# Kernel tuning notes

Hardware: AMD Instinct MI355X
Metric: run time of the kernel (lower is better)

The kernel has to match this reference:

```python
import jax, jax.numpy as jnp
import numpy as np

# SSMBlock constants (from init_kwargs and standard mamba_ssm defaults)
W = 8            # pooled spatial edge; d_model = W^3
K = 16           # AvgPool3d kernel & stride
D_MODEL = W ** 3            # 512
D_STATE = 16
EXPAND = 2
D_INNER = EXPAND * D_MODEL  # 1024
DT_RANK = D_MODEL // 16     # 32 (ceil(512/16))
D_CONV = 4


def setup_inputs() -> dict:
    key = jax.random.key(0)
    ks = jax.random.split(key, 8)
    s = 0.02
    x = jax.random.normal(ks[0], (1, 64, 128, 128, 128), dtype=jnp.float32)
    in_proj_w = jax.random.normal(ks[1], (2 * D_INNER, D_MODEL), jnp.float32) * s
    conv_w = jax.random.normal(ks[2], (D_INNER, D_CONV), jnp.float32) * s
    conv_b = jnp.zeros((D_INNER,), jnp.float32)
    x_proj_w = jax.random.normal(ks[3], (DT_RANK + 2 * D_STATE, D_INNER), jnp.float32) * s
    dt_proj_w = jax.random.normal(ks[4], (D_INNER, DT_RANK), jnp.float32) * s
    dt_proj_b = jax.random.uniform(ks[5], (D_INNER,), jnp.float32, minval=-4.0, maxval=-2.0)
    A_log = jnp.log(jnp.broadcast_to(jnp.arange(1, D_STATE + 1, dtype=jnp.float32), (D_INNER, D_STATE)))
    D = jnp.ones((D_INNER,), jnp.float32)
    out_proj_w = jax.random.normal(ks[6], (D_MODEL, D_INNER), jnp.float32) * s
    return dict(x=x, in_proj_w=in_proj_w, conv_w=conv_w, conv_b=conv_b,
                x_proj_w=x_proj_w, dt_proj_w=dt_proj_w, dt_proj_b=dt_proj_b,
                A_log=A_log, D=D, out_proj_w=out_proj_w)


def _forward(x, in_proj_w, conv_w, conv_b, x_proj_w, dt_proj_w, dt_proj_b, A_log, D, out_proj_w):
    B, C = x.shape[0], x.shape[1]
    # AvgPool3d(K, stride=K): non-overlapping -> reshape + mean
    xp = x.reshape(B, C, W, K, W, K, W, K).mean(axis=(3, 5, 7))  # (B,C,W,W,W)
    seq = xp.reshape(B, C, D_MODEL)  # Mamba input: L = C, d_model = W^3

    # in_proj -> (x, z)
    xz = jnp.einsum('bld,ed->ble', seq, in_proj_w)  # (B,L,2*D_INNER)
    xs, z = jnp.split(xz, 2, axis=-1)

    # causal depthwise conv1d along L + SiLU
    xt = jnp.pad(xs, ((0, 0), (D_CONV - 1, 0), (0, 0))).transpose(0, 2, 1)  # (B,E,L+pad)
    conv = jax.lax.conv_general_dilated(
        xt, conv_w[:, None, :], window_strides=(1,), padding='VALID',
        dimension_numbers=('NCH', 'OIH', 'NCH'), feature_group_count=D_INNER)
    xs = jax.nn.silu(conv.transpose(0, 2, 1) + conv_b)  # (B,L,E)

    # input-dependent dt, B, C
    x_dbl = jnp.einsum('ble,fe->blf', xs, x_proj_w)
    dt, Bs, Cs = jnp.split(x_dbl, [DT_RANK, DT_RANK + D_STATE], axis=-1)
    dt = jax.nn.softplus(jnp.einsum('blr,er->ble', dt, dt_proj_w) + dt_proj_b)  # (B,L,E)

    # selective scan: h_t = exp(dt*A) h_{t-1} + (dt*x) B_t ; y_t = <h_t, C_t> + D*x_t
    A = -jnp.exp(A_log)                                  # (E,S)
    dA = jnp.exp(dt[..., None] * A)                      # (B,L,E,S)
    dBx = (dt * xs)[..., None] * Bs[:, :, None, :]       # (B,L,E,S)

    def step(h, inp):
        da, dbx, c = inp
        h = da * h + dbx                                 # (B,E,S)
        y = jnp.einsum('bes,bs->be', h, c)
        return h, y

    h0 = jnp.zeros((B, D_INNER, D_STATE), xs.dtype)
    _, ys = jax.lax.scan(step, h0, (dA.transpose(1, 0, 2, 3), dBx.transpose(1, 0, 2, 3), Cs.transpose(1, 0, 2)))
    y = ys.transpose(1, 0, 2) + xs * D                   # (B,L,E)

    y = y * jax.nn.silu(z)
    out = jnp.einsum('ble,de->bld', y, out_proj_w)       # (B,L,d_model)
    return out.reshape(B, C, W, W, W)


def reference(x, in_proj_w, conv_w, conv_b, x_proj_w, dt_proj_w, dt_proj_b, A_log, D, out_proj_w):
    return _forward(x, in_proj_w, conv_w, conv_b, x_proj_w, dt_proj_w, dt_proj_b, A_log, D, out_proj_w)
```

## Files before the change

kernel.cpp:

```cpp
#include <hip/hip_runtime.h>
#include <math.h>

typedef float f32x4 __attribute__((ext_vector_type(4)));

__device__ __forceinline__ float dot4v(f32x4 a, f32x4 b){
    return a.x*b.x + a.y*b.y + a.z*b.z + a.w*b.w;
}
__device__ __forceinline__ float dot4(float4 a, float4 b){
    return a.x*b.x + a.y*b.y + a.z*b.z + a.w*b.w;
}

__device__ __forceinline__ float reduce4(float a0, float a1, float a2, float a3, int lane){
    int b0 = lane & 1, b1 = lane & 2;
    float r  = b0 ? a1 : a0;
    float rt = b0 ? a0 : a1;
    r += __shfl_xor(rt, 1);
    float s  = b0 ? a3 : a2;
    float st = b0 ? a2 : a3;
    s += __shfl_xor(st, 1);
    float u  = b1 ? s : r;
    float ut = b1 ? r : s;
    u += __shfl_xor(ut, 2);
    u += __shfl_xor(u, 4);
    u += __shfl_xor(u, 8);
    u += __shfl_xor(u, 16);
    u += __shfl_xor(u, 32);
    return u;
}

__global__ __launch_bounds__(256) void pool_k(const float* __restrict__ x,
                                              float* __restrict__ seq){
    __shared__ float red[4][8];
    int tid  = threadIdx.x;
    int lane = tid & 63;
    int part = tid >> 6;
    int cdh  = blockIdx.x;
    int c  = cdh >> 6;
    int od = (cdh >> 3) & 7;
    int oh = cdh & 7;
    int half = lane >> 5;
    int f    = lane & 31;

    const f32x4* px = (const f32x4*)x;
    size_t base = ((size_t)(c * 128 + od * 16) * 128 + (size_t)(oh * 16 + half)) * 32 + f
                + (size_t)part * 4 * 4096;

    float acc = 0.f;
    #pragma unroll
    for (int ii = 0; ii < 4; ii++){
        size_t o = base + (size_t)ii * 4096;
        #pragma unroll
        for (int jj = 0; jj < 8; jj++){
            f32x4 v = __builtin_nontemporal_load(&px[o + (size_t)jj * 64]);
            acc += (v.x + v.y) + (v.z + v.w);
        }
    }
    acc += __shfl_xor(acc, 1);
    acc += __shfl_xor(acc, 2);
    acc += __shfl_xor(acc, 32);
    if (lane < 32 && (lane & 3) == 0) red[part][lane >> 2] = acc;
    __syncthreads();
    if (tid < 8){
        float v = red[0][tid] + red[1][tid] + red[2][tid] + red[3][tid];
        seq[c * 512 + od * 64 + oh * 8 + tid] = v * (1.0f / 4096.0f);
    }
}

__global__ __launch_bounds__(256) void inproj_k(const float* __restrict__ seq,
                                                const float* __restrict__ Win,
                                                float* __restrict__ xz){
    int lane = threadIdx.x & 63;
    int wid  = blockIdx.x * 4 + (threadIdx.x >> 6);
    int l0 = (wid >> 8) << 4;
    int e0 = (wid & 255) << 3;
    const f32x4* S = (const f32x4*)seq;
    f32x4 sa[16], sb[16];
    #pragma unroll
    for (int r = 0; r < 16; r++){
        sa[r] = S[(size_t)(l0 + r) * 128 + lane];
        sb[r] = S[(size_t)(l0 + r) * 128 + lane + 64];
    }
    #pragma unroll 2
    for (int j = 0; j < 8; j++){
        int e = e0 + j;
        const f32x4* W = (const f32x4*)Win + (size_t)e * 128;
        f32x4 w0 = W[lane], w1 = W[lane + 64];
        float a[16];
        #pragma unroll
        for (int r = 0; r < 16; r++) a[r] = dot4v(w0, sa[r]) + dot4v(w1, sb[r]);
        float u0 = reduce4(a[0],  a[1],  a[2],  a[3],  lane);
        float u1 = reduce4(a[4],  a[5],  a[6],  a[7],  lane);
        float u2 = reduce4(a[8],  a[9],  a[10], a[11], lane);
        float u3 = reduce4(a[12], a[13], a[14], a[15], lane);
        if (lane < 4){
            xz[(size_t)(l0 + lane) * 2048 + e]      = u0;
            xz[(size_t)(l0 + 4  + lane) * 2048 + e] = u1;
            xz[(size_t)(l0 + 8  + lane) * 2048 + e] = u2;
            xz[(size_t)(l0 + 12 + lane) * 2048 + e] = u3;
        }
    }
}

__global__ __launch_bounds__(256) void xpc_k(const float* __restrict__ xz,
                                             const float* __restrict__ cw,
                                             const float* __restrict__ cb,
                                             const float* __restrict__ Wx,
                                             float* __restrict__ xsT,
                                             float* __restrict__ zsT,
                                             float* __restrict__ bcT,
                                             float* __restrict__ xdT){
    __shared__ float xs_row[1024];
    int bid = blockIdx.x;
    int l  = bid >> 2;
    int fg = bid & 3;
    int t  = threadIdx.x;

    #pragma unroll
    for (int j = 0; j < 4; j++){
        int e = t + j * 256;
        float v = cb[e];
        #pragma unroll
        for (int tt = 0; tt < 4; tt++){
            int ll = l - 3 + tt;
            if (ll >= 0) v += cw[e * 4 + tt] * xz[(size_t)ll * 2048 + e];
        }
        v = v / (1.f + expf(-v));
        xs_row[e] = v;
        if (fg == 0){
            xsT[(size_t)e * 64 + l] = v;
            float zv = xz[(size_t)l * 2048 + 1024 + e];
            zsT[(size_t)e * 64 + l] = zv / (1.f + expf(-zv));
        }
    }
    __syncthreads();

    int f = fg * 16 + (t >> 4);
    int q = t & 15;
    const float4* X  = (const float4*)xs_row;
    const float4* W4 = (const float4*)(Wx + (size_t)f * 1024);
    float acc = 0.f;
    #pragma unroll
    for (int k4 = 0; k4 < 16; k4++){
        int idx = q * 16 + k4;
        acc += dot4(X[idx], W4[idx]);
    }
    acc += __shfl_xor(acc, 1);
    acc += __shfl_xor(acc, 2);
    acc += __shfl_xor(acc, 4);
    acc += __shfl_xor(acc, 8);
    if (q == 0){
        if (f < 32) xdT[(size_t)f * 64 + l] = acc;
        else        bcT[(size_t)(f - 32) * 64 + l] = acc;
    }
}

__global__ __launch_bounds__(256) void scan_k(const float* __restrict__ xdT,
                                              const float* __restrict__ bcT,
                                              const float* __restrict__ xsT,
                                              const float* __restrict__ zsT,
                                              const float* __restrict__ Wdt,
                                              const float* __restrict__ bdt,
                                              const float* __restrict__ A_log,
                                              const float* __restrict__ Dv,
                                              float* __restrict__ y){
    __shared__ float red[4][64];
    int e    = blockIdx.x;
    int lane = threadIdx.x & 63;
    int w    = threadIdx.x >> 6;

    float acc = bdt[e];
    #pragma unroll 8
    for (int k = 0; k < 32; k++) acc += xdT[k * 64 + lane] * Wdt[e * 32 + k];
    float dtv = (acc > 20.f) ? acc : log1pf(expf(acc));
    float xv  = xsT[(size_t)e * 64 + lane];

    float py = 0.f;
    #pragma unroll
    for (int i = 0; i < 4; i++){
        int s = w * 4 + i;
        float A = -expf(A_log[e * 16 + s]);
        float a = expf(dtv * A);
        float b = (dtv * xv) * bcT[s * 64 + lane];
        #pragma unroll
        for (int d = 1; d < 64; d <<= 1){
            float ap = __shfl_up(a, d);
            float bp = __shfl_up(b, d);
            if (lane >= d){ b += a * bp; a *= ap; }
        }
        py += b * bcT[(16 + s) * 64 + lane];
    }
    red[w][lane] = py;
    __syncthreads();
    if (threadIdx.x < 64){
        float tot = red[0][lane] + red[1][lane] + red[2][lane] + red[3][lane];
        float yv = (tot + xv * Dv[e]) * zsT[(size_t)e * 64 + lane];
        y[(size_t)lane * 1024 + e] = yv;
    }
}

__global__ __launch_bounds__(256) void outproj_k(const float* __restrict__ y,
                                                 const float* __restrict__ Wo,
                                                 float* __restrict__ out){
    int lane = threadIdx.x & 63;
    int wid  = blockIdx.x * 4 + (threadIdx.x >> 6);
    int l0 = (wid >> 6) << 3;
    int d0 = (wid & 63) << 3;
    const f32x4* Y = (const f32x4*)y;
    f32x4 yr[8][4];
    #pragma unroll
    for (int r = 0; r < 8; r++){
        #pragma unroll
        for (int q = 0; q < 4; q++)
            yr[r][q] = Y[(size_t)(l0 + r) * 256 + q * 64 + lane];
    }
    #pragma unroll 2
    for (int j = 0; j < 8; j++){
        int d = d0 + j;
        const f32x4* W = (const f32x4*)Wo + (size_t)d * 256;
        float a[8] = {0,0,0,0,0,0,0,0};
        #pragma unroll
        for (int q = 0; q < 4; q++){
            f32x4 w = W[q * 64 + lane];
            #pragma unroll
            for (int r = 0; r < 8; r++) a[r] += dot4v(w, yr[r][q]);
        }
        float u0 = reduce4(a[0], a[1], a[2], a[3], lane);
        float u1 = reduce4(a[4], a[5], a[6], a[7], lane);
        if (lane < 4){
            out[(size_t)(l0 + lane) * 512 + d]     = u0;
            out[(size_t)(l0 + 4 + lane) * 512 + d] = u1;
        }
    }
}

extern "C" void kernel_launch(void* const* d_in, const int* in_sizes, int n_in,
                              void* d_out, int out_size, void* d_ws, size_t ws_size,
                              hipStream_t stream){
    const float* x          = (const float*)d_in[0];
    const float* in_proj_w  = (const float*)d_in[1];
    const float* conv_w     = (const float*)d_in[2];
    const float* conv_b     = (const float*)d_in[3];
    const float* x_proj_w   = (const float*)d_in[4];
    const float* dt_proj_w  = (const float*)d_in[5];
    const float* dt_proj_b  = (const float*)d_in[6];
    const float* A_log      = (const float*)d_in[7];
    const float* Dv         = (const float*)d_in[8];
    const float* out_proj_w = (const float*)d_in[9];
    float* out = (float*)d_out;

    float* ws   = (float*)d_ws;
    float* seq  = ws;
    float* xz   = ws + 32768;
    float* xsT  = ws + 163840;
    float* zsT  = ws + 229376;
    float* bcT  = ws + 294912;
    float* xdT  = ws + 296960;
    float* y    = ws + 299008;

    hipLaunchKernelGGL(pool_k,    dim3(4096), dim3(256), 0, stream, x, seq);
    hipLaunchKernelGGL(inproj_k,  dim3(256),  dim3(256), 0, stream, seq, in_proj_w, xz);
    hipLaunchKernelGGL(xpc_k,     dim3(256),  dim3(256), 0, stream, xz, conv_w, conv_b,
                       x_proj_w, xsT, zsT, bcT, xdT);
    hipLaunchKernelGGL(scan_k,    dim3(1024), dim3(256), 0, stream, xdT, bcT, xsT, zsT,
                       dt_proj_w, dt_proj_b, A_log, Dv, y);
    hipLaunchKernelGGL(outproj_k, dim3(128),  dim3(256), 0, stream, y, out_proj_w, out);
}
```

Baseline: 123.6 us.

## Fuse in_proj, causal conv, SiLU and x_proj into one kernel with atomics

Merges the in_proj and conv/x_proj kernels into a single kernel. Each block computes an 8-column slice of xz for all 64 positions and keeps it in shared memory, so the full xz round trip through global memory and one launch go away. The block then applies the conv and SiLU and adds its partial x_proj contributions through atomicAdd into a buffer that pool_k zeroes. The cost is many float atomics and a reduction order that is no longer deterministic. The z-half blocks sit idle during the x_proj phase.

```diff
diff --git a/kernel.cpp b/kernel.cpp
--- a/kernel.cpp
+++ b/kernel.cpp
@@ -29,12 +29,17 @@
 }
 
 __global__ __launch_bounds__(256) void pool_k(const float* __restrict__ x,
-                                              float* __restrict__ seq){
+                                              float* __restrict__ seq,
+                                              float* __restrict__ xd){
     __shared__ float red[4][8];
     int tid  = threadIdx.x;
     int lane = tid & 63;
     int part = tid >> 6;
     int cdh  = blockIdx.x;
+    if (cdh == 0){
+        #pragma unroll
+        for (int i = 0; i < 16; i++) xd[tid + i * 256] = 0.f;
+    }
     int c  = cdh >> 6;
     int od = (cdh >> 3) & 7;
     int oh = cdh & 7;
@@ -66,96 +71,97 @@
     }
 }
 
-__global__ __launch_bounds__(256) void inproj_k(const float* __restrict__ seq,
-                                                const float* __restrict__ Win,
-                                                float* __restrict__ xz){
-    int lane = threadIdx.x & 63;
-    int wid  = blockIdx.x * 4 + (threadIdx.x >> 6);
-    int l0 = (wid >> 8) << 4;
-    int e0 = (wid & 255) << 3;
-    const f32x4* S = (const f32x4*)seq;
-    f32x4 sa[16], sb[16];
-    #pragma unroll
-    for (int r = 0; r < 16; r++){
-        sa[r] = S[(size_t)(l0 + r) * 128 + lane];
-        sb[r] = S[(size_t)(l0 + r) * 128 + lane + 64];
-    }
-    #pragma unroll 2
-    for (int j = 0; j < 8; j++){
-        int e = e0 + j;
-        const f32x4* W = (const f32x4*)Win + (size_t)e * 128;
-        f32x4 w0 = W[lane], w1 = W[lane + 64];
-        float a[16];
-        #pragma unroll
-        for (int r = 0; r < 16; r++) a[r] = dot4v(w0, sa[r]) + dot4v(w1, sb[r]);
-        float u0 = reduce4(a[0],  a[1],  a[2],  a[3],  lane);
-        float u1 = reduce4(a[4],  a[5],  a[6],  a[7],  lane);
-        float u2 = reduce4(a[8],  a[9],  a[10], a[11], lane);
-        float u3 = reduce4(a[12], a[13], a[14], a[15], lane);
-        if (lane < 4){
-            xz[(size_t)(l0 + lane) * 2048 + e]      = u0;
-            xz[(size_t)(l0 + 4  + lane) * 2048 + e] = u1;
-            xz[(size_t)(l0 + 8  + lane) * 2048 + e] = u2;
-            xz[(size_t)(l0 + 12 + lane) * 2048 + e] = u3;
-        }
-    }
-}
-
-__global__ __launch_bounds__(256) void xpc_k(const float* __restrict__ xz,
-                                             const float* __restrict__ cw,
-                                             const float* __restrict__ cb,
-                                             const float* __restrict__ Wx,
-                                             float* __restrict__ xsT,
-                                             float* __restrict__ zsT,
-                                             float* __restrict__ bcT,
-                                             float* __restrict__ xdT){
-    __shared__ float xs_row[1024];
-    int bid = blockIdx.x;
-    int l  = bid >> 2;
-    int fg = bid & 3;
-    int t  = threadIdx.x;
-
-    #pragma unroll
-    for (int j = 0; j < 4; j++){
-        int e = t + j * 256;
-        float v = cb[e];
-        #pragma unroll
-        for (int tt = 0; tt < 4; tt++){
-            int ll = l - 3 + tt;
-            if (ll >= 0) v += cw[e * 4 + tt] * xz[(size_t)ll * 2048 + e];
-        }
-        v = v / (1.f + expf(-v));
-        xs_row[e] = v;
-        if (fg == 0){
+__global__ __launch_bounds__(256) void fused_k(const float* __restrict__ seq,
+                                               const float* __restrict__ Win,
+                                               const float* __restrict__ cw,
+                                               const float* __restrict__ cb,
+                                               const float* __restrict__ Wx,
+                                               float* __restrict__ xsT,
+                                               float* __restrict__ zsT,
+                                               float* __restrict__ xd){
+    __shared__ float xzt[64][9];
+    __shared__ float xst[64][9];
+    int t    = threadIdx.x;
+    int lane = t & 63;
+    int w    = t >> 6;
+    int e0   = blockIdx.x * 8;
+    int l0   = w * 16;
+
+    {
+        const f32x4* S = (const f32x4*)seq;
+        f32x4 sa[16], sb[16];
+        #pragma unroll
+        for (int r = 0; r < 16; r++){
+            sa[r] = S[(size_t)(l0 + r) * 128 + lane];
+            sb[r] = S[(size_t)(l0 + r) * 128 + lane + 64];
+        }
+        #pragma unroll 2
+        for (int j = 0; j < 8; j++){
+            const f32x4* W = (const f32x4*)Win + (size_t)(e0 + j) * 128;
+            f32x4 w0 = W[lane], w1 = W[lane + 64];
+            float a[16];
+            #pragma unroll
+            for (int r = 0; r < 16; r++) a[r] = dot4v(w0, sa[r]) + dot4v(w1, sb[r]);
+            float u0 = reduce4(a[0],  a[1],  a[2],  a[3],  lane);
+            float u1 = reduce4(a[4],  a[5],  a[6],  a[7],  lane);
+            float u2 = reduce4(a[8],  a[9],  a[10], a[11], lane);
+            float u3 = reduce4(a[12], a[13], a[14], a[15], lane);
+            if (lane < 4){
+                xzt[l0 + lane][j]      = u0;
+                xzt[l0 + 4  + lane][j] = u1;
+                xzt[l0 + 8  + lane][j] = u2;
+                xzt[l0 + 12 + lane][j] = u3;
+            }
+        }
+    }
+    __syncthreads();
+
+    if (e0 < 1024){
+        #pragma unroll
+        for (int jj = 0; jj < 2; jj++){
+            int idx = t + jj * 256;
+            int l  = idx & 63;
+            int e8 = idx >> 6;
+            int e  = e0 + e8;
+            float v = cb[e];
+            #pragma unroll
+            for (int tt = 0; tt < 4; tt++){
+                int ll = l - 3 + tt;
+                if (ll >= 0) v += cw[e * 4 + tt] * xzt[ll][e8];
+            }
+            v = v / (1.f + expf(-v));
+            xst[l][e8] = v;
             xsT[(size_t)e * 64 + l] = v;
-            float zv = xz[(size_t)l * 2048 + 1024 + e];
-            zsT[(size_t)e * 64 + l] = zv / (1.f + expf(-zv));
-        }
-    }
-    __syncthreads();
-
-    int f = fg * 16 + (t >> 4);
-    int q = t & 15;
-    const float4* X  = (const float4*)xs_row;
-    const float4* W4 = (const float4*)(Wx + (size_t)f * 1024);
-    float acc = 0.f;
-    #pragma unroll
-    for (int k4 = 0; k4 < 16; k4++){
-        int idx = q * 16 + k4;
-        acc += dot4(X[idx], W4[idx]);
-    }
-    acc += __shfl_xor(acc, 1);
-    acc += __shfl_xor(acc, 2);
-    acc += __shfl_xor(acc, 4);
-    acc += __shfl_xor(acc, 8);
-    if (q == 0){
-        if (f < 32) xdT[(size_t)f * 64 + l] = acc;
-        else        bcT[(size_t)(f - 32) * 64 + l] = acc;
-    }
-}
-
-__global__ __launch_bounds__(256) void scan_k(const float* __restrict__ xdT,
-                                              const float* __restrict__ bcT,
+        }
+        __syncthreads();
+
+        int l  = t >> 2;
+        int fg = t & 3;
+        float xr[8];
+        #pragma unroll
+        for (int j = 0; j < 8; j++) xr[j] = xst[l][j];
+        #pragma unroll 4
+        for (int i = 0; i < 16; i++){
+            int f = fg * 16 + i;
+            const float* Wr = Wx + (size_t)f * 1024 + e0;
+            float p = 0.f;
+            #pragma unroll
+            for (int j = 0; j < 8; j++) p += xr[j] * Wr[j];
+            atomicAdd(&xd[f * 64 + l], p);
+        }
+    } else {
+        #pragma unroll
+        for (int jj = 0; jj < 2; jj++){
+            int idx = t + jj * 256;
+            int l  = idx & 63;
+            int e8 = idx >> 6;
+            float zv = xzt[l][e8];
+            zsT[(size_t)(e0 - 1024 + e8) * 64 + l] = zv / (1.f + expf(-zv));
+        }
+    }
+}
+
+__global__ __launch_bounds__(256) void scan_k(const float* __restrict__ xd,
                                               const float* __restrict__ xsT,
                                               const float* __restrict__ zsT,
                                               const float* __restrict__ Wdt,
@@ -164,13 +170,14 @@
                                               const float* __restrict__ Dv,
                                               float* __restrict__ y){
     __shared__ float red[4][64];
+    const float* bcT = xd + 2048;
     int e    = blockIdx.x;
     int lane = threadIdx.x & 63;
     int w    = threadIdx.x >> 6;
 
     float acc = bdt[e];
     #pragma unroll 8
-    for (int k = 0; k < 32; k++) acc += xdT[k * 64 + lane] * Wdt[e * 32 + k];
+    for (int k = 0; k < 32; k++) acc += xd[k * 64 + lane] * Wdt[e * 32 + k];
     float dtv = (acc > 20.f) ? acc : log1pf(expf(acc));
     float xv  = xsT[(size_t)e * 64 + lane];
 
@@ -250,18 +257,15 @@
 
     float* ws   = (float*)d_ws;
     float* seq  = ws;
-    float* xz   = ws + 32768;
-    float* xsT  = ws + 163840;
-    float* zsT  = ws + 229376;
-    float* bcT  = ws + 294912;
-    float* xdT  = ws + 296960;
-    float* y    = ws + 299008;
-
-    hipLaunchKernelGGL(pool_k,    dim3(4096), dim3(256), 0, stream, x, seq);
-    hipLaunchKernelGGL(inproj_k,  dim3(256),  dim3(256), 0, stream, seq, in_proj_w, xz);
-    hipLaunchKernelGGL(xpc_k,     dim3(256),  dim3(256), 0, stream, xz, conv_w, conv_b,
-                       x_proj_w, xsT, zsT, bcT, xdT);
-    hipLaunchKernelGGL(scan_k,    dim3(1024), dim3(256), 0, stream, xdT, bcT, xsT, zsT,
+    float* xsT  = ws + 32768;
+    float* zsT  = ws + 98304;
+    float* xd   = ws + 163840;
+    float* y    = ws + 167936;
+
+    hipLaunchKernelGGL(pool_k,    dim3(4096), dim3(256), 0, stream, x, seq, xd);
+    hipLaunchKernelGGL(fused_k,   dim3(256),  dim3(256), 0, stream, seq, in_proj_w,
+                       conv_w, conv_b, x_proj_w, xsT, zsT, xd);
+    hipLaunchKernelGGL(scan_k,    dim3(1024), dim3(256), 0, stream, xd, xsT, zsT,
                        dt_proj_w, dt_proj_b, A_log, Dv, y);
     hipLaunchKernelGGL(outproj_k, dim3(128),  dim3(256), 0, stream, y, out_proj_w, out);
 }
```

Measured after the change: 123.7 us (median of 2 runs). Within noise of the previous version (+0.1%).
